# Optimization experiments

Hardware: AMD Instinct MI355X
Metric: run time of the kernel (lower is better)

Reference implementation:

```python
import jax, jax.numpy as jnp
import numpy as np

HEADS = 8
LEVELS = 4
POINTS = 4
ED = 256
HD = ED // HEADS  # 32
SPATIAL = [[92, 92], [46, 46], [23, 23], [12, 12]]  # sum(H*W)=11253


def _linear_params(key, d_in, d_out):
    kw, kb = jax.random.split(key)
    W = jax.random.normal(kw, (d_in, d_out), jnp.float32) * 0.02
    b = jax.random.normal(kb, (d_out,), jnp.float32) * 0.02
    return W, b


def setup_inputs() -> dict:
    key = jax.random.key(0)
    ks = jax.random.split(key, 8)
    bs, nq = 2, sum(h * w for h, w in SPATIAL)
    W_val, b_val = _linear_params(ks[3], ED, ED)
    W_off, b_off = _linear_params(ks[4], ED, HEADS * LEVELS * POINTS * 2)
    W_attn, b_attn = _linear_params(ks[5], ED, HEADS * LEVELS * POINTS)
    W_out, b_out = _linear_params(ks[6], ED, ED)
    return {
        "query": jax.random.normal(ks[0], (bs, nq, ED), jnp.float32),
        "value": jax.random.normal(ks[1], (bs, nq, ED), jnp.float32),
        "reference_points": jax.random.uniform(ks[2], (bs, nq, LEVELS, 2), jnp.float32),
        "spatial_shapes": jnp.array(SPATIAL, dtype=jnp.int32),
        "W_val": W_val, "b_val": b_val,
        "W_off": W_off, "b_off": b_off,
        "W_attn": W_attn, "b_attn": b_attn,
        "W_out": W_out, "b_out": b_out,
    }


def _bilinear_sample(img, grid):
    # img: [B, H, W, D]; grid: [B, Q, P, 2] with (x, y) in [-1, 1]
    # matches torch grid_sample(mode='bilinear', padding_mode='zeros', align_corners=False)
    B, H, W, D = img.shape
    x = (grid[..., 0] + 1.0) * (W * 0.5) - 0.5
    y = (grid[..., 1] + 1.0) * (H * 0.5) - 0.5
    x0 = jnp.floor(x)
    y0 = jnp.floor(y)
    wx1 = x - x0
    wy1 = y - y0
    wx0 = 1.0 - wx1
    wy0 = 1.0 - wy1
    flat = img.reshape(B, H * W, D)

    def gather(xi, yi):
        valid = (xi >= 0) & (xi <= W - 1) & (yi >= 0) & (yi <= H - 1)
        xc = jnp.clip(xi, 0, W - 1).astype(jnp.int32)
        yc = jnp.clip(yi, 0, H - 1).astype(jnp.int32)
        idx = (yc * W + xc).reshape(B, -1)  # [B, Q*P]
        v = jnp.take_along_axis(flat, idx[..., None], axis=1)
        v = v.reshape(B, xi.shape[1], xi.shape[2], D)
        return v * valid[..., None].astype(img.dtype)

    v00 = gather(x0, y0)
    v01 = gather(x0 + 1, y0)
    v10 = gather(x0, y0 + 1)
    v11 = gather(x0 + 1, y0 + 1)
    return (v00 * (wx0 * wy0)[..., None] + v01 * (wx1 * wy0)[..., None]
            + v10 * (wx0 * wy1)[..., None] + v11 * (wx1 * wy1)[..., None])


def reference(query, value, reference_points, spatial_shapes,
              W_val, b_val, W_off, b_off, W_attn, b_attn, W_out, b_out):
    bs, nq, _ = query.shape
    identity = query

    v = (value @ W_val + b_val).reshape(bs, -1, HEADS, HD)
    offsets = (query @ W_off + b_off).reshape(bs, nq, HEADS, LEVELS, POINTS, 2)
    attn = jax.nn.softmax((query @ W_attn + b_attn).reshape(bs, nq, HEADS, LEVELS * POINTS), axis=-1)
    attn = attn.reshape(bs, nq, HEADS, LEVELS, POINTS)

    # normalizer is (W, H) per level
    norm = jnp.stack([spatial_shapes[:, 1], spatial_shapes[:, 0]], -1).astype(query.dtype)
    loc = reference_points[:, :, None, :, None, :] + offsets / norm[None, None, None, :, None, :]
    grids = 2.0 * loc - 1.0  # [bs, nq, HEADS, LEVELS, POINTS, 2]

    shapes = np.asarray(spatial_shapes).tolist()  # static per-level loop
    B = bs * HEADS
    samples = []
    start = 0
    for lvl, (H, W) in enumerate(shapes):
        vl = v[:, start:start + H * W]                       # [bs, HW, HEADS, HD]
        start += H * W
        img = vl.transpose(0, 2, 1, 3).reshape(B, H, W, HD)  # [B, H, W, HD]
        g = grids[:, :, :, lvl].transpose(0, 2, 1, 3, 4).reshape(B, nq, POINTS, 2)
        samples.append(_bilinear_sample(img, g))             # [B, nq, POINTS, HD]
    samp = jnp.stack(samples, axis=2)                        # [B, nq, LEVELS, POINTS, HD]

    w = attn.transpose(0, 2, 1, 3, 4).reshape(B, nq, LEVELS, POINTS)
    out = jnp.einsum('bqlpd,bqlp->bqd', samp, w)             # [B, nq, HD]
    out = out.reshape(bs, HEADS, nq, HD).transpose(0, 2, 1, 3).reshape(bs, nq, ED)
    out = out @ W_out + b_out
    return out + identity
```

## Files before the change

### kernel.cpp

```cpp
#include <hip/hip_runtime.h>
#include <hip/hip_bf16.h>
#include <math.h>

#define BS      2
#define NQ      11253
#define MROWS   (BS * NQ)
#define ED      256
#define HEADS   8
#define HD      32
#define LEVELS  4
#define POINTS  4
#define QPB     4

typedef __attribute__((ext_vector_type(8))) short  bf16x8_t;
typedef __attribute__((ext_vector_type(4))) float  f32x4_t;

__device__ __forceinline__ unsigned short f2bf(float f) {
    unsigned int u = __float_as_uint(f);
    u += 0x7FFFu + ((u >> 16) & 1u);
    return (unsigned short)(u >> 16);
}
__device__ __forceinline__ float bf2f(unsigned short h) {
    return __uint_as_float(((unsigned int)h) << 16);
}

__global__ __launch_bounds__(256) void prep_weight(
    const float* __restrict__ W, unsigned short* __restrict__ hi,
    unsigned short* __restrict__ lo, int N, int total)
{
    const int id = blockIdx.x * 256 + threadIdx.x;
    if (id >= total) return;
    const int n = id >> 8;
    const int k = id & 255;
    const float f = W[(size_t)k * N + n];
    const unsigned short h = f2bf(f);
    const unsigned short l = f2bf(f - bf2f(h));
    hi[(size_t)n * 256 + k] = h;
    lo[(size_t)n * 256 + k] = l;
}

__global__ __launch_bounds__(256) void gemm_mfma_split(
    const float* __restrict__ A,
    const unsigned short* __restrict__ Bth,
    const unsigned short* __restrict__ Btl,
    const float* __restrict__ bias,
    const float* __restrict__ bias2,
    const float* __restrict__ res,
    float* __restrict__ C,
    int M, int N, int nsplit)
{
    __shared__ __align__(16) unsigned short As_hi[2][128][32];
    __shared__ __align__(16) unsigned short As_lo[2][128][32];
    __shared__ __align__(16) unsigned short Bs_hi[2][64][32];
    __shared__ __align__(16) unsigned short Bs_lo[2][64][32];

    const int tid  = threadIdx.x;
    const int wave = tid >> 6, lane = tid & 63;
    const int l15  = lane & 15, kg = lane >> 4;
    const int row0 = blockIdx.y * 128;
    const int col0 = blockIdx.x * 64;
    const int wr   = (wave >> 1) * 64;
    const int wc   = (wave & 1) * 32;
    const int arow = tid >> 1, ak = (tid & 1) * 16;
    const int brow = tid >> 2, bk = (tid & 3) * 8;

    float4   aR[4];
    bf16x8_t bRh, bRl;

    auto stage_load = [&](int k0) {
        const int r = row0 + arow;
        if (r < M) {
            const float4* ap = (const float4*)&A[(size_t)r * 256 + k0 + ak];
            aR[0] = ap[0]; aR[1] = ap[1]; aR[2] = ap[2]; aR[3] = ap[3];
        } else {
            aR[0] = aR[1] = aR[2] = aR[3] = make_float4(0.f, 0.f, 0.f, 0.f);
        }
        const size_t bb = (size_t)(col0 + brow) * 256 + k0 + bk;
        bRh = *(const bf16x8_t*)&Bth[bb];
        bRl = *(const bf16x8_t*)&Btl[bb];
    };

    auto stage_write = [&](int buf) {
        float t[16];
        *(float4*)&t[0]  = aR[0]; *(float4*)&t[4]  = aR[1];
        *(float4*)&t[8]  = aR[2]; *(float4*)&t[12] = aR[3];
        bf16x8_t h0, l0, h1, l1;
        #pragma unroll
        for (int i = 0; i < 8; ++i) {
            unsigned short h = f2bf(t[i]);
            h0[i] = (short)h; l0[i] = (short)f2bf(t[i] - bf2f(h));
        }
        #pragma unroll
        for (int i = 0; i < 8; ++i) {
            unsigned short h = f2bf(t[8 + i]);
            h1[i] = (short)h; l1[i] = (short)f2bf(t[8 + i] - bf2f(h));
        }
        *(bf16x8_t*)&As_hi[buf][arow][ak]     = h0;
        *(bf16x8_t*)&As_hi[buf][arow][ak + 8] = h1;
        *(bf16x8_t*)&As_lo[buf][arow][ak]     = l0;
        *(bf16x8_t*)&As_lo[buf][arow][ak + 8] = l1;
        *(bf16x8_t*)&Bs_hi[buf][brow][bk] = bRh;
        *(bf16x8_t*)&Bs_lo[buf][brow][bk] = bRl;
    };

    f32x4_t acc[4][2];
    #pragma unroll
    for (int i = 0; i < 4; ++i)
        #pragma unroll
        for (int j = 0; j < 2; ++j)
            acc[i][j] = (f32x4_t){0.f, 0.f, 0.f, 0.f};

    stage_load(0);
    stage_write(0);
    __syncthreads();

    for (int s = 0; s < 8; ++s) {
        const int buf = s & 1;
        if (s < 7) stage_load((s + 1) * 32);

        bf16x8_t ah[4], al[4], bh[2], bl[2];
        #pragma unroll
        for (int mi = 0; mi < 4; ++mi) {
            ah[mi] = *(const bf16x8_t*)&As_hi[buf][wr + mi * 16 + l15][kg * 8];
            al[mi] = *(const bf16x8_t*)&As_lo[buf][wr + mi * 16 + l15][kg * 8];
        }
        #pragma unroll
        for (int nj = 0; nj < 2; ++nj) {
            bh[nj] = *(const bf16x8_t*)&Bs_hi[buf][wc + nj * 16 + l15][kg * 8];
            bl[nj] = *(const bf16x8_t*)&Bs_lo[buf][wc + nj * 16 + l15][kg * 8];
        }
        #pragma unroll
        for (int mi = 0; mi < 4; ++mi)
            #pragma unroll
            for (int nj = 0; nj < 2; ++nj) {
                acc[mi][nj] = __builtin_amdgcn_mfma_f32_16x16x32_bf16(
                    ah[mi], bh[nj], acc[mi][nj], 0, 0, 0);
                acc[mi][nj] = __builtin_amdgcn_mfma_f32_16x16x32_bf16(
                    ah[mi], bl[nj], acc[mi][nj], 0, 0, 0);
                acc[mi][nj] = __builtin_amdgcn_mfma_f32_16x16x32_bf16(
                    al[mi], bh[nj], acc[mi][nj], 0, 0, 0);
            }

        if (s < 7) stage_write(buf ^ 1);
        __syncthreads();
    }

    #pragma unroll
    for (int nj = 0; nj < 2; ++nj) {
        const int c = col0 + wc + nj * 16 + l15;
        const float bi = (c < nsplit) ? bias[c] : bias2[c - nsplit];
        #pragma unroll
        for (int mi = 0; mi < 4; ++mi) {
            const int rb = row0 + wr + mi * 16 + kg * 4;
            #pragma unroll
            for (int j = 0; j < 4; ++j) {
                const int r = rb + j;
                if (r < M) {
                    float o = acc[mi][nj][j] + bi;
                    if (res) o += res[(size_t)r * N + c];
                    C[(size_t)r * N + c] = o;
                }
            }
        }
    }
}

__global__ __launch_bounds__(256) void msda_sample_kernel(
    const float* __restrict__ v,
    const float* __restrict__ cat,
    const float* __restrict__ refp,
    float* __restrict__ out)
{
    const int q0  = blockIdx.x * QPB;
    const int tid = threadIdx.x;

    __shared__ float s_in[QPB][384];
    __shared__ float s_ref[QPB][8];
    __shared__ __align__(16) float s_w[QPB][16][HEADS][4];
    __shared__ __align__(16) int   s_o[QPB][16][HEADS][4];

    for (int i = tid; i < QPB * 384; i += 256) {
        const int q = i / 384, j = i - q * 384;
        const int qq = q0 + q;
        s_in[q][j] = (qq < MROWS) ? cat[(size_t)qq * 384 + j] : 0.f;
    }
    if (tid < QPB * 8) {
        const int q = tid >> 3, j = tid & 7;
        const int qq = q0 + q;
        s_ref[q][j] = (qq < MROWS) ? refp[(size_t)qq * 8 + j] : 0.5f;
    }
    __syncthreads();

    #pragma unroll
    for (int rep = 0; rep < 2; ++rep) {
        const int u  = rep * 256 + tid;
        const int p  = u & 15;
        const int gh = u >> 4;
        const int q  = gh >> 3, h = gh & 7;
        const int lvl = p >> 2;

        const float logit = s_in[q][256 + h * 16 + p];
        float mx = logit;
        #pragma unroll
        for (int m = 1; m < 16; m <<= 1) mx = fmaxf(mx, __shfl_xor(mx, m, 16));
        const float e = __expf(logit - mx);
        float sum = e;
        #pragma unroll
        for (int m = 1; m < 16; m <<= 1) sum += __shfl_xor(sum, m, 16);
        const float w = e / sum;

        const int   Wd = (lvl == 0) ? 92 : (lvl == 1) ? 46 : (lvl == 2) ? 23 : 12;
        const int   s0 = (lvl == 0) ? 0  : (lvl == 1) ? 8464 : (lvl == 2) ? 10580 : 11109;
        const float Wf = (float)Wd;

        const float x = s_ref[q][lvl * 2 + 0] * Wf + s_in[q][h * 32 + p * 2 + 0] - 0.5f;
        const float y = s_ref[q][lvl * 2 + 1] * Wf + s_in[q][h * 32 + p * 2 + 1] - 0.5f;
        const float x0f = floorf(x), y0f = floorf(y);
        const int   x0 = (int)x0f,  y0 = (int)y0f;
        const float wx1 = x - x0f, wy1 = y - y0f;
        const float wx0 = 1.f - wx1, wy0 = 1.f - wy1;

        const bool vx0 = (x0 >= 0) & (x0 < Wd);
        const bool vx1 = (x0 >= -1) & (x0 < Wd - 1);
        const bool vy0 = (y0 >= 0) & (y0 < Wd);
        const bool vy1 = (y0 >= -1) & (y0 < Wd - 1);

        const int xc0 = min(max(x0, 0), Wd - 1);
        const int xc1 = min(max(x0 + 1, 0), Wd - 1);
        const int yc0 = min(max(y0, 0), Wd - 1);
        const int yc1 = min(max(y0 + 1, 0), Wd - 1);

        const int hb = h * HD;
        const int r0 = (s0 + yc0 * Wd) * ED + hb;
        const int r1 = (s0 + yc1 * Wd) * ED + hb;

        s_w[q][p][h][0] = (vx0 & vy0) ? w * wx0 * wy0 : 0.f;
        s_w[q][p][h][1] = (vx1 & vy0) ? w * wx1 * wy0 : 0.f;
        s_w[q][p][h][2] = (vx0 & vy1) ? w * wx0 * wy1 : 0.f;
        s_w[q][p][h][3] = (vx1 & vy1) ? w * wx1 * wy1 : 0.f;
        s_o[q][p][h][0] = r0 + xc0 * ED;
        s_o[q][p][h][1] = r0 + xc1 * ED;
        s_o[q][p][h][2] = r1 + xc0 * ED;
        s_o[q][p][h][3] = r1 + xc1 * ED;
    }
    __syncthreads();

    const int q  = tid >> 6, l = tid & 63;
    const int h  = l >> 3,  c4 = (l & 7) * 4;
    const int qq = q0 + q;
    const int qc = (qq < MROWS) ? qq : MROWS - 1;
    const int b  = qc / NQ;
    const float* __restrict__ vb = v + (size_t)b * NQ * ED + c4;

    float4 acc = make_float4(0.f, 0.f, 0.f, 0.f);
    #pragma unroll
    for (int p = 0; p < 16; p += 2) {
        const float4 wA = *(const float4*)&s_w[q][p][h][0];
        const int4   oA = *(const int4*)&s_o[q][p][h][0];
        const float4 wB = *(const float4*)&s_w[q][p + 1][h][0];
        const int4   oB = *(const int4*)&s_o[q][p + 1][h][0];
        const float4 a0 = *(const float4*)&vb[oA.x];
        const float4 a1 = *(const float4*)&vb[oA.y];
        const float4 a2 = *(const float4*)&vb[oA.z];
        const float4 a3 = *(const float4*)&vb[oA.w];
        const float4 b0 = *(const float4*)&vb[oB.x];
        const float4 b1 = *(const float4*)&vb[oB.y];
        const float4 b2 = *(const float4*)&vb[oB.z];
        const float4 b3 = *(const float4*)&vb[oB.w];
        acc.x = fmaf(wA.x, a0.x, acc.x); acc.y = fmaf(wA.x, a0.y, acc.y);
        acc.z = fmaf(wA.x, a0.z, acc.z); acc.w = fmaf(wA.x, a0.w, acc.w);
        acc.x = fmaf(wA.y, a1.x, acc.x); acc.y = fmaf(wA.y, a1.y, acc.y);
        acc.z = fmaf(wA.y, a1.z, acc.z); acc.w = fmaf(wA.y, a1.w, acc.w);
        acc.x = fmaf(wA.z, a2.x, acc.x); acc.y = fmaf(wA.z, a2.y, acc.y);
        acc.z = fmaf(wA.z, a2.z, acc.z); acc.w = fmaf(wA.z, a2.w, acc.w);
        acc.x = fmaf(wA.w, a3.x, acc.x); acc.y = fmaf(wA.w, a3.y, acc.y);
        acc.z = fmaf(wA.w, a3.z, acc.z); acc.w = fmaf(wA.w, a3.w, acc.w);
        acc.x = fmaf(wB.x, b0.x, acc.x); acc.y = fmaf(wB.x, b0.y, acc.y);
        acc.z = fmaf(wB.x, b0.z, acc.z); acc.w = fmaf(wB.x, b0.w, acc.w);
        acc.x = fmaf(wB.y, b1.x, acc.x); acc.y = fmaf(wB.y, b1.y, acc.y);
        acc.z = fmaf(wB.y, b1.z, acc.z); acc.w = fmaf(wB.y, b1.w, acc.w);
        acc.x = fmaf(wB.z, b2.x, acc.x); acc.y = fmaf(wB.z, b2.y, acc.y);
        acc.z = fmaf(wB.z, b2.z, acc.z); acc.w = fmaf(wB.z, b2.w, acc.w);
        acc.x = fmaf(wB.w, b3.x, acc.x); acc.y = fmaf(wB.w, b3.y, acc.y);
        acc.z = fmaf(wB.w, b3.z, acc.z); acc.w = fmaf(wB.w, b3.w, acc.w);
    }
    if (qq < MROWS)
        *(float4*)&out[(size_t)qq * ED + h * HD + c4] = acc;
}

extern "C" void kernel_launch(void* const* d_in, const int* in_sizes, int n_in,
                              void* d_out, int out_size, void* d_ws, size_t ws_size,
                              hipStream_t stream) {
    const float* query = (const float*)d_in[0];
    const float* value = (const float*)d_in[1];
    const float* refp  = (const float*)d_in[2];
    const float* W_val  = (const float*)d_in[4];
    const float* b_val  = (const float*)d_in[5];
    const float* W_off  = (const float*)d_in[6];
    const float* b_off  = (const float*)d_in[7];
    const float* W_attn = (const float*)d_in[8];
    const float* b_attn = (const float*)d_in[9];
    const float* W_out  = (const float*)d_in[10];
    const float* b_out  = (const float*)d_in[11];
    float* out = (float*)d_out;

    float* ws      = (float*)d_ws;
    float* v_ws    = ws;
    float* cat_ws  = v_ws   + (size_t)MROWS * 256;
    float* msda_ws = cat_ws + (size_t)MROWS * 384;
    unsigned short* wsu = (unsigned short*)(msda_ws + (size_t)MROWS * 256);
    unsigned short* wv_hi = wsu;
    unsigned short* wv_lo = wv_hi + 65536;
    unsigned short* wc_hi = wv_lo + 65536;
    unsigned short* wc_lo = wc_hi + 98304;
    unsigned short* wu_hi = wc_lo + 98304;
    unsigned short* wu_lo = wu_hi + 65536;

    dim3 blk(256);

    hipLaunchKernelGGL(prep_weight, dim3(256), blk, 0, stream,
                       W_val, wv_hi, wv_lo, 256, 65536);
    hipLaunchKernelGGL(prep_weight, dim3(256), blk, 0, stream,
                       W_off, wc_hi, wc_lo, 256, 65536);
    hipLaunchKernelGGL(prep_weight, dim3(128), blk, 0, stream,
                       W_attn, wc_hi + 65536, wc_lo + 65536, 128, 32768);
    hipLaunchKernelGGL(prep_weight, dim3(256), blk, 0, stream,
                       W_out, wu_hi, wu_lo, 256, 65536);

    const int MB = (MROWS + 127) / 128;
    hipLaunchKernelGGL(gemm_mfma_split, dim3(4, MB), blk, 0, stream,
                       value, wv_hi, wv_lo, b_val, (const float*)nullptr,
                       (const float*)nullptr, v_ws, MROWS, 256, 256);
    hipLaunchKernelGGL(gemm_mfma_split, dim3(6, MB), blk, 0, stream,
                       query, wc_hi, wc_lo, b_off, b_attn,
                       (const float*)nullptr, cat_ws, MROWS, 384, 256);
    hipLaunchKernelGGL(msda_sample_kernel, dim3((MROWS + QPB - 1) / QPB), blk,
                       0, stream, v_ws, cat_ws, refp, msda_ws);
    hipLaunchKernelGGL(gemm_mfma_split, dim3(4, MB), blk, 0, stream,
                       msda_ws, wu_hi, wu_lo, b_out, (const float*)nullptr,
                       query, out, MROWS, 256, 256);
}
```

Before: 263.2 us.

## Pre-split activations to bf16 hi/lo and store intermediates in bf16

Adds a prep_act kernel that splits value and query into bf16 hi/lo pairs ahead of the GEMMs, so the GEMM staging loop no longer converts fp32 per tile. The value projection and offset/attention projection now write bf16 outputs, which halves the bytes read by the gather-heavy sampling kernel. The sampling kernel writes its result directly as hi/lo bf16 for the output GEMM. The cost is two extra passes over the activations, plus reduced precision in the sampled values and offsets, which can shift sampling locations and affect accuracy.

```diff
diff --git a/kernel.cpp b/kernel.cpp
--- a/kernel.cpp
+++ b/kernel.cpp
@@ -8,9 +8,8 @@
 #define ED      256
 #define HEADS   8
 #define HD      32
-#define LEVELS  4
-#define POINTS  4
 #define QPB     4
+#define M256    ((size_t)MROWS * 256)
 
 typedef __attribute__((ext_vector_type(8))) short  bf16x8_t;
 typedef __attribute__((ext_vector_type(4))) float  f32x4_t;
@@ -39,14 +38,36 @@
     lo[(size_t)n * 256 + k] = l;
 }
 
-__global__ __launch_bounds__(256) void gemm_mfma_split(
-    const float* __restrict__ A,
+__global__ __launch_bounds__(256) void prep_act(
+    const float* __restrict__ X, unsigned short* __restrict__ hi,
+    unsigned short* __restrict__ lo, int total8)
+{
+    const int id = blockIdx.x * 256 + threadIdx.x;
+    if (id >= total8) return;
+    const float4* p = (const float4*)(X + (size_t)id * 8);
+    const float4 a = p[0], b = p[1];
+    const float t[8] = {a.x, a.y, a.z, a.w, b.x, b.y, b.z, b.w};
+    bf16x8_t h, l;
+    #pragma unroll
+    for (int i = 0; i < 8; ++i) {
+        const unsigned short hh = f2bf(t[i]);
+        h[i] = (short)hh;
+        l[i] = (short)f2bf(t[i] - bf2f(hh));
+    }
+    *(bf16x8_t*)(hi + (size_t)id * 8) = h;
+    *(bf16x8_t*)(lo + (size_t)id * 8) = l;
+}
+
+__global__ __launch_bounds__(256) void gemm_mfma_pre(
+    const unsigned short* __restrict__ Ah,
+    const unsigned short* __restrict__ Al,
     const unsigned short* __restrict__ Bth,
     const unsigned short* __restrict__ Btl,
     const float* __restrict__ bias,
     const float* __restrict__ bias2,
     const float* __restrict__ res,
-    float* __restrict__ C,
+    float* __restrict__ Cf,
+    unsigned short* __restrict__ Cbf,
     int M, int N, int nsplit)
 {
     __shared__ __align__(16) unsigned short As_hi[2][128][32];
@@ -64,16 +85,18 @@
     const int arow = tid >> 1, ak = (tid & 1) * 16;
     const int brow = tid >> 2, bk = (tid & 3) * 8;
 
-    float4   aR[4];
-    bf16x8_t bRh, bRl;
+    bf16x8_t aRh[2], aRl[2], bRh, bRl;
 
     auto stage_load = [&](int k0) {
         const int r = row0 + arow;
         if (r < M) {
-            const float4* ap = (const float4*)&A[(size_t)r * 256 + k0 + ak];
-            aR[0] = ap[0]; aR[1] = ap[1]; aR[2] = ap[2]; aR[3] = ap[3];
+            const size_t ab = (size_t)r * 256 + k0 + ak;
+            aRh[0] = *(const bf16x8_t*)&Ah[ab];
+            aRh[1] = *(const bf16x8_t*)&Ah[ab + 8];
+            aRl[0] = *(const bf16x8_t*)&Al[ab];
+            aRl[1] = *(const bf16x8_t*)&Al[ab + 8];
         } else {
-            aR[0] = aR[1] = aR[2] = aR[3] = make_float4(0.f, 0.f, 0.f, 0.f);
+            aRh[0] = aRh[1] = aRl[0] = aRl[1] = (bf16x8_t)(short)0;
         }
         const size_t bb = (size_t)(col0 + brow) * 256 + k0 + bk;
         bRh = *(const bf16x8_t*)&Bth[bb];
@@ -81,24 +104,10 @@
     };
 
     auto stage_write = [&](int buf) {
-        float t[16];
-        *(float4*)&t[0]  = aR[0]; *(float4*)&t[4]  = aR[1];
-        *(float4*)&t[8]  = aR[2]; *(float4*)&t[12] = aR[3];
-        bf16x8_t h0, l0, h1, l1;
-        #pragma unroll
-        for (int i = 0; i < 8; ++i) {
-            unsigned short h = f2bf(t[i]);
-            h0[i] = (short)h; l0[i] = (short)f2bf(t[i] - bf2f(h));
-        }
-        #pragma unroll
-        for (int i = 0; i < 8; ++i) {
-            unsigned short h = f2bf(t[8 + i]);
-            h1[i] = (short)h; l1[i] = (short)f2bf(t[8 + i] - bf2f(h));
-        }
-        *(bf16x8_t*)&As_hi[buf][arow][ak]     = h0;
-        *(bf16x8_t*)&As_hi[buf][arow][ak + 8] = h1;
-        *(bf16x8_t*)&As_lo[buf][arow][ak]     = l0;
-        *(bf16x8_t*)&As_lo[buf][arow][ak + 8] = l1;
+        *(bf16x8_t*)&As_hi[buf][arow][ak]     = aRh[0];
+        *(bf16x8_t*)&As_hi[buf][arow][ak + 8] = aRh[1];
+        *(bf16x8_t*)&As_lo[buf][arow][ak]     = aRl[0];
+        *(bf16x8_t*)&As_lo[buf][arow][ak + 8] = aRl[1];
         *(bf16x8_t*)&Bs_hi[buf][brow][bk] = bRh;
         *(bf16x8_t*)&Bs_lo[buf][brow][bk] = bRl;
     };
@@ -157,8 +166,12 @@
                 const int r = rb + j;
                 if (r < M) {
                     float o = acc[mi][nj][j] + bi;
-                    if (res) o += res[(size_t)r * N + c];
-                    C[(size_t)r * N + c] = o;
+                    if (Cbf) {
+                        Cbf[(size_t)r * N + c] = f2bf(o);
+                    } else {
+                        if (res) o += res[(size_t)r * N + c];
+                        Cf[(size_t)r * N + c] = o;
+                    }
                 }
             }
         }
@@ -166,10 +179,11 @@
 }
 
 __global__ __launch_bounds__(256) void msda_sample_kernel(
-    const float* __restrict__ v,
-    const float* __restrict__ cat,
+    const unsigned short* __restrict__ v,
+    const unsigned short* __restrict__ cat,
     const float* __restrict__ refp,
-    float* __restrict__ out)
+    unsigned short* __restrict__ out_hi,
+    unsigned short* __restrict__ out_lo)
 {
     const int q0  = blockIdx.x * QPB;
     const int tid = threadIdx.x;
@@ -182,7 +196,7 @@
     for (int i = tid; i < QPB * 384; i += 256) {
         const int q = i / 384, j = i - q * 384;
         const int qq = q0 + q;
-        s_in[q][j] = (qq < MROWS) ? cat[(size_t)qq * 384 + j] : 0.f;
+        s_in[q][j] = (qq < MROWS) ? bf2f(cat[(size_t)qq * 384 + j]) : 0.f;
     }
     if (tid < QPB * 8) {
         const int q = tid >> 3, j = tid & 7;
@@ -250,7 +264,7 @@
     const int qq = q0 + q;
     const int qc = (qq < MROWS) ? qq : MROWS - 1;
     const int b  = qc / NQ;
-    const float* __restrict__ vb = v + (size_t)b * NQ * ED + c4;
+    const unsigned short* __restrict__ vb = v + (size_t)b * NQ * ED + c4;
 
     float4 acc = make_float4(0.f, 0.f, 0.f, 0.f);
     #pragma unroll
@@ -259,33 +273,41 @@
         const int4   oA = *(const int4*)&s_o[q][p][h][0];
         const float4 wB = *(const float4*)&s_w[q][p + 1][h][0];
         const int4   oB = *(const int4*)&s_o[q][p + 1][h][0];
-        const float4 a0 = *(const float4*)&vb[oA.x];
-        const float4 a1 = *(const float4*)&vb[oA.y];
-        const float4 a2 = *(const float4*)&vb[oA.z];
-        const float4 a3 = *(const float4*)&vb[oA.w];
-        const float4 b0 = *(const float4*)&vb[oB.x];
-        const float4 b1 = *(const float4*)&vb[oB.y];
-        const float4 b2 = *(const float4*)&vb[oB.z];
-        const float4 b3 = *(const float4*)&vb[oB.w];
-        acc.x = fmaf(wA.x, a0.x, acc.x); acc.y = fmaf(wA.x, a0.y, acc.y);
-        acc.z = fmaf(wA.x, a0.z, acc.z); acc.w = fmaf(wA.x, a0.w, acc.w);
-        acc.x = fmaf(wA.y, a1.x, acc.x); acc.y = fmaf(wA.y, a1.y, acc.y);
-        acc.z = fmaf(wA.y, a1.z, acc.z); acc.w = fmaf(wA.y, a1.w, acc.w);
-        acc.x = fmaf(wA.z, a2.x, acc.x); acc.y = fmaf(wA.z, a2.y, acc.y);
-        acc.z = fmaf(wA.z, a2.z, acc.z); acc.w = fmaf(wA.z, a2.w, acc.w);
-        acc.x = fmaf(wA.w, a3.x, acc.x); acc.y = fmaf(wA.w, a3.y, acc.y);
-        acc.z = fmaf(wA.w, a3.z, acc.z); acc.w = fmaf(wA.w, a3.w, acc.w);
-        acc.x = fmaf(wB.x, b0.x, acc.x); acc.y = fmaf(wB.x, b0.y, acc.y);
-        acc.z = fmaf(wB.x, b0.z, acc.z); acc.w = fmaf(wB.x, b0.w, acc.w);
-        acc.x = fmaf(wB.y, b1.x, acc.x); acc.y = fmaf(wB.y, b1.y, acc.y);
-        acc.z = fmaf(wB.y, b1.z, acc.z); acc.w = fmaf(wB.y, b1.w, acc.w);
-        acc.x = fmaf(wB.z, b2.x, acc.x); acc.y = fmaf(wB.z, b2.y, acc.y);
-        acc.z = fmaf(wB.z, b2.z, acc.z); acc.w = fmaf(wB.z, b2.w, acc.w);
-        acc.x = fmaf(wB.w, b3.x, acc.x); acc.y = fmaf(wB.w, b3.y, acc.y);
-        acc.z = fmaf(wB.w, b3.z, acc.z); acc.w = fmaf(wB.w, b3.w, acc.w);
-    }
-    if (qq < MROWS)
-        *(float4*)&out[(size_t)qq * ED + h * HD + c4] = acc;
+        const ushort4 u0 = *(const ushort4*)&vb[oA.x];
+        const ushort4 u1 = *(const ushort4*)&vb[oA.y];
+        const ushort4 u2 = *(const ushort4*)&vb[oA.z];
+        const ushort4 u3 = *(const ushort4*)&vb[oA.w];
+        const ushort4 u4 = *(const ushort4*)&vb[oB.x];
+        const ushort4 u5 = *(const ushort4*)&vb[oB.y];
+        const ushort4 u6 = *(const ushort4*)&vb[oB.z];
+        const ushort4 u7 = *(const ushort4*)&vb[oB.w];
+        acc.x = fmaf(wA.x, bf2f(u0.x), acc.x); acc.y = fmaf(wA.x, bf2f(u0.y), acc.y);
+        acc.z = fmaf(wA.x, bf2f(u0.z), acc.z); acc.w = fmaf(wA.x, bf2f(u0.w), acc.w);
+        acc.x = fmaf(wA.y, bf2f(u1.x), acc.x); acc.y = fmaf(wA.y, bf2f(u1.y), acc.y);
+        acc.z = fmaf(wA.y, bf2f(u1.z), acc.z); acc.w = fmaf(wA.y, bf2f(u1.w), acc.w);
+        acc.x = fmaf(wA.z, bf2f(u2.x), acc.x); acc.y = fmaf(wA.z, bf2f(u2.y), acc.y);
+        acc.z = fmaf(wA.z, bf2f(u2.z), acc.z); acc.w = fmaf(wA.z, bf2f(u2.w), acc.w);
+        acc.x = fmaf(wA.w, bf2f(u3.x), acc.x); acc.y = fmaf(wA.w, bf2f(u3.y), acc.y);
+        acc.z = fmaf(wA.w, bf2f(u3.z), acc.z); acc.w = fmaf(wA.w, bf2f(u3.w), acc.w);
+        acc.x = fmaf(wB.x, bf2f(u4.x), acc.x); acc.y = fmaf(wB.x, bf2f(u4.y), acc.y);
+        acc.z = fmaf(wB.x, bf2f(u4.z), acc.z); acc.w = fmaf(wB.x, bf2f(u4.w), acc.w);
+        acc.x = fmaf(wB.y, bf2f(u5.x), acc.x); acc.y = fmaf(wB.y, bf2f(u5.y), acc.y);
+        acc.z = fmaf(wB.y, bf2f(u5.z), acc.z); acc.w = fmaf(wB.y, bf2f(u5.w), acc.w);
+        acc.x = fmaf(wB.z, bf2f(u6.x), acc.x); acc.y = fmaf(wB.z, bf2f(u6.y), acc.y);
+        acc.z = fmaf(wB.z, bf2f(u6.z), acc.z); acc.w = fmaf(wB.z, bf2f(u6.w), acc.w);
+        acc.x = fmaf(wB.w, bf2f(u7.x), acc.x); acc.y = fmaf(wB.w, bf2f(u7.y), acc.y);
+        acc.z = fmaf(wB.w, bf2f(u7.z), acc.z); acc.w = fmaf(wB.w, bf2f(u7.w), acc.w);
+    }
+    if (qq < MROWS) {
+        ushort4 oh, ol;
+        oh.x = f2bf(acc.x); ol.x = f2bf(acc.x - bf2f(oh.x));
+        oh.y = f2bf(acc.y); ol.y = f2bf(acc.y - bf2f(oh.y));
+        oh.z = f2bf(acc.z); ol.z = f2bf(acc.z - bf2f(oh.z));
+        oh.w = f2bf(acc.w); ol.w = f2bf(acc.w - bf2f(oh.w));
+        const size_t ob = (size_t)qq * ED + h * HD + c4;
+        *(ushort4*)&out_hi[ob] = oh;
+        *(ushort4*)&out_lo[ob] = ol;
+    }
 }
 
 extern "C" void kernel_launch(void* const* d_in, const int* in_sizes, int n_in,
@@ -304,12 +326,14 @@
     const float* b_out  = (const float*)d_in[11];
     float* out = (float*)d_out;
 
-    float* ws      = (float*)d_ws;
-    float* v_ws    = ws;
-    float* cat_ws  = v_ws   + (size_t)MROWS * 256;
-    float* msda_ws = cat_ws + (size_t)MROWS * 384;
-    unsigned short* wsu = (unsigned short*)(msda_ws + (size_t)MROWS * 256);
-    unsigned short* wv_hi = wsu;
+    unsigned short* u = (unsigned short*)d_ws;
+    unsigned short* a1_hi = u;
+    unsigned short* a1_lo = a1_hi + M256;
+    unsigned short* q_hi  = a1_lo + M256;
+    unsigned short* q_lo  = q_hi + M256;
+    unsigned short* v_bf  = q_lo + M256;
+    unsigned short* cat_bf = v_bf + M256;
+    unsigned short* wv_hi = cat_bf + (size_t)MROWS * 384;
     unsigned short* wv_lo = wv_hi + 65536;
     unsigned short* wc_hi = wv_lo + 65536;
     unsigned short* wc_lo = wc_hi + 98304;
@@ -327,16 +351,26 @@
     hipLaunchKernelGGL(prep_weight, dim3(256), blk, 0, stream,
                        W_out, wu_hi, wu_lo, 256, 65536);
 
+    const int total8 = (int)(M256 / 8);
+    const int pgrid  = (total8 + 255) / 256;
+    hipLaunchKernelGGL(prep_act, dim3(pgrid), blk, 0, stream,
+                       value, a1_hi, a1_lo, total8);
+    hipLaunchKernelGGL(prep_act, dim3(pgrid), blk, 0, stream,
+                       query, q_hi, q_lo, total8);
+
     const int MB = (MROWS + 127) / 128;
-    hipLaunchKernelGGL(gemm_mfma_split, dim3(4, MB), blk, 0, stream,
-                       value, wv_hi, wv_lo, b_val, (const float*)nullptr,
-                       (const float*)nullptr, v_ws, MROWS, 256, 256);
-    hipLaunchKernelGGL(gemm_mfma_split, dim3(6, MB), blk, 0, stream,
-                       query, wc_hi, wc_lo, b_off, b_attn,
-                       (const float*)nullptr, cat_ws, MROWS, 384, 256);
+    hipLaunchKernelGGL(gemm_mfma_pre, dim3(4, MB), blk, 0, stream,
+                       a1_hi, a1_lo, wv_hi, wv_lo, b_val, (const float*)nullptr,
+                       (const float*)nullptr, (float*)nullptr, v_bf,
+                       MROWS, 256, 256);
+    hipLaunchKernelGGL(gemm_mfma_pre, dim3(6, MB), blk, 0, stream,
+                       q_hi, q_lo, wc_hi, wc_lo, b_off, b_attn,
+                       (const float*)nullptr, (float*)nullptr, cat_bf,
+                       MROWS, 384, 256);
     hipLaunchKernelGGL(msda_sample_kernel, dim3((MROWS + QPB - 1) / QPB), blk,
-                       0, stream, v_ws, cat_ws, refp, msda_ws);
-    hipLaunchKernelGGL(gemm_mfma_split, dim3(4, MB), blk, 0, stream,
-                       msda_ws, wu_hi, wu_lo, b_out, (const float*)nullptr,
-                       query, out, MROWS, 256, 256);
-}
+                       0, stream, v_bf, cat_bf, refp, a1_hi, a1_lo);
+    hipLaunchKernelGGL(gemm_mfma_pre, dim3(4, MB), blk, 0, stream,
+                       a1_hi, a1_lo, wu_hi, wu_lo, b_out, (const float*)nullptr,
+                       query, out, (unsigned short*)nullptr,
+                       MROWS, 256, 256);
+}
```

Result: slower. 274.7 us (+4.4%).
